# Kernel tuning notes

Measured on AMD Instinct MI355X. Metric: run time of the kernel, lower is better.

## Reference

```python
import jax, jax.numpy as jnp
import numpy as np

N = 4096
K = 64
E = N * K
LD = 2      # location_dim
ED = 8      # attention embed_dim
H = 256     # lck_structure width
BN_EPS = 1e-5


def setup_inputs() -> dict:
    key = jax.random.key(0)
    ks = jax.random.split(key, 12)
    coor = jax.random.normal(ks[0], (E, 2 * LD), dtype=jnp.float32)
    row = jnp.repeat(jnp.arange(N, dtype=jnp.int64), K)
    col = jax.random.randint(ks[1], (E,), 0, N, dtype=jnp.int64)
    sparse_idx = jnp.stack([row, col], axis=0)
    geodesic = jax.random.uniform(ks[2], (N, N), dtype=jnp.float32)
    angle_ratio = jax.random.uniform(ks[3], (N, N), dtype=jnp.float32)
    # LocalConditionalKer params: Linear(4,H), Linear(H,H), BN(H), Linear(H,1)
    W0 = jax.random.normal(ks[4], (2 * LD, H), dtype=jnp.float32) / np.sqrt(2 * LD)
    b0 = jnp.zeros((H,), jnp.float32)
    W1 = jax.random.normal(ks[5], (H, H), dtype=jnp.float32) / np.sqrt(H)
    b1 = jnp.zeros((H,), jnp.float32)
    gamma = jnp.ones((H,), jnp.float32)
    beta = jnp.zeros((H,), jnp.float32)
    W2 = jax.random.normal(ks[6], (H, 1), dtype=jnp.float32) / np.sqrt(H)
    b2 = jnp.zeros((1,), jnp.float32)
    # Attention params: query/key Linear(LD, ED)
    Wq = jax.random.normal(ks[7], (LD, ED), dtype=jnp.float32) / np.sqrt(LD)
    bq = jnp.zeros((ED,), jnp.float32)
    Wk = jax.random.normal(ks[8], (LD, ED), dtype=jnp.float32) / np.sqrt(LD)
    bk = jnp.zeros((ED,), jnp.float32)
    x = jax.random.normal(ks[9], (1,), dtype=jnp.float32)
    return dict(x=x, coor=coor, sparse_idx=sparse_idx, geodesic=geodesic,
                angle_ratio=angle_ratio, W0=W0, b0=b0, W1=W1, b1=b1,
                gamma=gamma, beta=beta, W2=W2, b2=b2,
                Wq=Wq, bq=bq, Wk=Wk, bk=bk)


def _lck(coor, W0, b0, W1, b1, gamma, beta, W2, b2):
    # loop semantics: activation applied before every layer except j==1
    h = jnp.tanh(coor) @ W0 + b0          # j=0: Linear(4,H)
    h = h @ W1 + b1                        # j=1: Linear(H,H), no pre-activation
    h = jnp.tanh(h)                        # j=2: BN(H) in training mode (batch stats)
    mu = jnp.mean(h, axis=0)
    var = jnp.var(h, axis=0)               # biased variance, as torch BN uses
    h = gamma * (h - mu) * jax.lax.rsqrt(var + BN_EPS) + beta
    h = jnp.tanh(h) @ W2 + b2              # j=3: Linear(H,1)
    return jax.nn.relu(h)                  # [E,1]


def reference(x, coor, sparse_idx, geodesic, angle_ratio,
              W0, b0, W1, b1, gamma, beta, W2, b2, Wq, bq, Wk, bk):
    row, col = sparse_idx[0], sparse_idx[1]
    # per-edge kernel value, scattered into dense NxN (duplicates summed)
    vals = _lck(coor, W0, b0, W1, b1, gamma, beta, W2, b2).reshape(-1)  # [E]
    lcker = jnp.zeros((N, N), vals.dtype).at[row, col].add(vals)
    # attention over neighbors
    sphere = coor[:, :LD] + coor[:, LD:]           # [E, 2]
    sphere = sphere.reshape(N, K, LD)               # [N, K, 2]
    center = sphere[:, :1, :]                       # [N, 1, 2]
    q = center @ Wq + bq                            # [N, 1, ED]
    k = sphere @ Wk + bk                            # [N, K, ED]
    att = jnp.abs(jnp.einsum('nqe,nke->nqk', q, k).squeeze(1))  # [N, K]
    alpha = jnp.zeros((N, N), att.dtype).at[row, col].add(att.reshape(-1))
    distance_decay = jnp.exp(-alpha * geodesic)
    return lcker * distance_decay * angle_ratio
```

## Files before the change

kernel.cpp:

```cpp
#include <hip/hip_runtime.h>

#define N_ 4096
#define K_ 64
#define E_ (N_*K_)
#define H_ 256
#define EPS_ 1e-5f
#define L2E_ 1.4426950408889634f
#define TL2E_ 2.8853900817779268f

#if __has_builtin(__builtin_amdgcn_exp2f)
#define EXP2(x) __builtin_amdgcn_exp2f(x)
#else
#define EXP2(x) __expf((x) * 0.6931471805599453f)
#endif

__device__ __forceinline__ float ftanh(float x) {
    float e = EXP2(x * TL2E_);
    return 1.0f - 2.0f * __builtin_amdgcn_rcpf(e + 1.0f);
}

__global__ __launch_bounds__(256) void prep_kernel(
    const float* __restrict__ W0, const float* __restrict__ b0,
    const float* __restrict__ W1, const float* __restrict__ b1,
    float* __restrict__ W01, float* __restrict__ b01)
{
    int c = threadIdx.x;
    int h0 = blockIdx.x * 8;
    float a0 = 0.f, a1 = 0.f, a2 = 0.f, a3 = 0.f, ab = 0.f;
    #pragma unroll
    for (int h = h0; h < h0 + 8; ++h) {
        float w = W1[h * H_ + c];
        a0 = fmaf(W0[0 * H_ + h], w, a0);
        a1 = fmaf(W0[1 * H_ + h], w, a1);
        a2 = fmaf(W0[2 * H_ + h], w, a2);
        a3 = fmaf(W0[3 * H_ + h], w, a3);
        ab = fmaf(b0[h], w, ab);
    }
    if (blockIdx.x == 0) ab += b1[c];
    atomicAdd(&W01[c], a0);
    atomicAdd(&W01[H_ + c], a1);
    atomicAdd(&W01[2 * H_ + c], a2);
    atomicAdd(&W01[3 * H_ + c], a3);
    atomicAdd(&b01[c], ab);
}

__global__ __launch_bounds__(256, 8) void stats_kernel(
    const float* __restrict__ coor, const float* __restrict__ W01,
    const float* __restrict__ b01, float* __restrict__ part)
{
    const int c = threadIdx.x;
    const float w0 = TL2E_ * W01[c],        w1 = TL2E_ * W01[H_ + c];
    const float w2 = TL2E_ * W01[2*H_ + c], w3 = TL2E_ * W01[3*H_ + c];
    const float bb = TL2E_ * b01[c];
    __shared__ float4 T[128];
    const int e0 = blockIdx.x * 128;
    if (c < 128) {
        float4 v = reinterpret_cast<const float4*>(coor)[e0 + c];
        T[c] = make_float4(ftanh(v.x), ftanh(v.y), ftanh(v.z), ftanh(v.w));
    }
    __syncthreads();
    float sr = 0.f, sr2 = 0.f;
    #pragma unroll 8
    for (int i = 0; i < 128; ++i) {
        float4 t = T[i];
        float u = fmaf(t.w, w3, fmaf(t.z, w2, fmaf(t.y, w1, fmaf(t.x, w0, bb))));
        float r = __builtin_amdgcn_rcpf(EXP2(u) + 1.0f);
        sr += r;
        sr2 = fmaf(r, r, sr2);
    }
    part[blockIdx.x * 512 + c] = sr;
    part[blockIdx.x * 512 + 256 + c] = sr2;
}

__global__ __launch_bounds__(512) void reduce_kernel(
    const float* __restrict__ part, float* __restrict__ sums)
{
    int t = threadIdx.x;
    int b0 = blockIdx.x * 64;
    float local = 0.f;
    #pragma unroll 8
    for (int b = b0; b < b0 + 64; ++b) local += part[b * 512 + t];
    atomicAdd(&sums[t], local);
}

__global__ __launch_bounds__(256) void finalize_kernel(
    const float* __restrict__ sums, const float* __restrict__ gamma,
    const float* __restrict__ beta, const float* __restrict__ W2,
    const float* __restrict__ b2,
    const float* __restrict__ W01, const float* __restrict__ b01,
    float* __restrict__ folded, float* __restrict__ swp)
{
    int c = threadIdx.x;
    const float inv = 1.0f / (float)E_;
    float p = sums[c] * inv;
    float q = sums[256 + c] * inv;
    float mu = 1.0f - 2.0f * p;
    float var = 4.0f * fmaf(-p, p, q);
    float a = gamma[c] * rsqrtf(var + EPS_);
    float bf = fmaf(-mu, a, beta[c]);
    folded[c * 8 + 0] = TL2E_ * W01[c];
    folded[c * 8 + 1] = TL2E_ * W01[H_ + c];
    folded[c * 8 + 2] = TL2E_ * W01[2 * H_ + c];
    folded[c * 8 + 3] = TL2E_ * W01[3 * H_ + c];
    folded[c * 8 + 4] = TL2E_ * b01[c];
    folded[c * 8 + 5] = -4.0f * L2E_ * a;
    folded[c * 8 + 6] = TL2E_ * (a + bf);
    folded[c * 8 + 7] = -2.0f * W2[c];
    __shared__ float red[256];
    red[c] = W2[c];
    __syncthreads();
    for (int s = 128; s > 0; s >>= 1) {
        if (c < s) red[c] += red[c + s];
        __syncthreads();
    }
    if (c == 0) swp[0] = red[0] + b2[0];
}

__global__ __launch_bounds__(256, 8) void edge_kernel(
    const float* __restrict__ coor, const int* __restrict__ idx,
    const float* __restrict__ folded, const float* __restrict__ swp,
    const float* __restrict__ Wq, const float* __restrict__ bq,
    const float* __restrict__ Wk, const float* __restrict__ bk,
    const float* __restrict__ geo, const float* __restrict__ ang,
    float* __restrict__ out)
{
    __shared__ float4 FS[2 * H_ + 16];
    __shared__ float  TSx[128], TSy[128], TSz[128], TSw[128];
    __shared__ float  ACC[16][128];
    __shared__ int    COL[128];
    __shared__ float  ATT[128];

    const int t = threadIdx.x;
    const int row0 = blockIdx.x * 2;
    const int eb0 = blockIdx.x * 128;

    {
        const float4* F = reinterpret_cast<const float4*>(folded);
        FS[t + (t >> 5)] = F[t];
        int j = t + 256;
        FS[j + (j >> 5)] = F[j];
    }
    int col = 0;
    if (t < 128) {
        float4 ce = reinterpret_cast<const float4*>(coor)[eb0 + t];
        TSx[t] = ftanh(ce.x); TSy[t] = ftanh(ce.y);
        TSz[t] = ftanh(ce.z); TSw[t] = ftanh(ce.w);
        col = idx[E_ + eb0 + t];
        float ex = ce.x + ce.z, ey = ce.y + ce.w;
        float sx = __shfl(ex, 0), sy = __shfl(ey, 0);
        float att = 0.f;
        #pragma unroll
        for (int j = 0; j < 8; ++j) {
            float qj = fmaf(sy, Wq[8 + j], fmaf(sx, Wq[j], bq[j]));
            float kj = fmaf(ey, Wk[8 + j], fmaf(ex, Wk[j], bk[j]));
            att = fmaf(qj, kj, att);
        }
        COL[t] = col;
        ATT[t] = fabsf(att);
    }
    {
        float4 z = make_float4(0.f, 0.f, 0.f, 0.f);
        float4* orow = reinterpret_cast<float4*>(out + (size_t)row0 * N_);
        #pragma unroll
        for (int i = 0; i < 8; ++i) orow[i * 256 + t] = z;
    }
    __syncthreads();

    const int eg = (t & 15) * 8;
    const int chunk = t >> 4;
    float4 xa = *reinterpret_cast<const float4*>(&TSx[eg]);
    float4 xb = *reinterpret_cast<const float4*>(&TSx[eg + 4]);
    float4 ya = *reinterpret_cast<const float4*>(&TSy[eg]);
    float4 yb = *reinterpret_cast<const float4*>(&TSy[eg + 4]);
    float4 za = *reinterpret_cast<const float4*>(&TSz[eg]);
    float4 zb = *reinterpret_cast<const float4*>(&TSz[eg + 4]);
    float4 wa = *reinterpret_cast<const float4*>(&TSw[eg]);
    float4 wb = *reinterpret_cast<const float4*>(&TSw[eg + 4]);
    const float4* Fp = &FS[chunk * 33];
    float ac0 = 0.f, ac1 = 0.f, ac2 = 0.f, ac3 = 0.f;
    float ac4 = 0.f, ac5 = 0.f, ac6 = 0.f, ac7 = 0.f;
    #define EVAL(tx_, ty_, tz_, tw_, ak) { \
        float u = fmaf(tw_, f0.w, fmaf(tz_, f0.z, fmaf(ty_, f0.y, fmaf(tx_, f0.x, f1.x)))); \
        float r = __builtin_amdgcn_rcpf(EXP2(u) + 1.0f); \
        float r2 = __builtin_amdgcn_rcpf(EXP2(fmaf(r, f1.y, f1.z)) + 1.0f); \
        ak = fmaf(r2, f1.w, ak); }
    #pragma unroll 4
    for (int i = 0; i < 16; ++i) {
        float4 f0 = Fp[2 * i];
        float4 f1 = Fp[2 * i + 1];
        EVAL(xa.x, ya.x, za.x, wa.x, ac0)
        EVAL(xa.y, ya.y, za.y, wa.y, ac1)
        EVAL(xa.z, ya.z, za.z, wa.z, ac2)
        EVAL(xa.w, ya.w, za.w, wa.w, ac3)
        EVAL(xb.x, yb.x, zb.x, wb.x, ac4)
        EVAL(xb.y, yb.y, zb.y, wb.y, ac5)
        EVAL(xb.z, yb.z, zb.z, wb.z, ac6)
        EVAL(xb.w, yb.w, zb.w, wb.w, ac7)
    }
    #undef EVAL
    *reinterpret_cast<float4*>(&ACC[chunk][eg])     = make_float4(ac0, ac1, ac2, ac3);
    *reinterpret_cast<float4*>(&ACC[chunk][eg + 4]) = make_float4(ac4, ac5, ac6, ac7);
    __syncthreads();

    const int w = t >> 6, lane = t & 63;
    if (w < 2) {
        float val = swp[0];
        #pragma unroll
        for (int c = 0; c < 16; ++c) val += ACC[c][t];
        val = fmaxf(val, 0.f);

        size_t p = (size_t)(row0 + w) * N_ + col;
        float g = geo[p], an = ang[p];

        const int rb = w * 64;
        unsigned long long m = 0;
        float asum = 0.f;
        #pragma unroll 8
        for (int j4 = 0; j4 < 16; ++j4) {
            int4   c4 = *reinterpret_cast<const int4*>(&COL[rb + 4 * j4]);
            float4 a4 = *reinterpret_cast<const float4*>(&ATT[rb + 4 * j4]);
            m |= (unsigned long long)(c4.x == col) << (4 * j4 + 0);
            m |= (unsigned long long)(c4.y == col) << (4 * j4 + 1);
            m |= (unsigned long long)(c4.z == col) << (4 * j4 + 2);
            m |= (unsigned long long)(c4.w == col) << (4 * j4 + 3);
            asum += (c4.x == col) ? a4.x : 0.f;
            asum += (c4.y == col) ? a4.y : 0.f;
            asum += (c4.z == col) ? a4.z : 0.f;
            asum += (c4.w == col) ? a4.w : 0.f;
        }
        bool leader = ((m & ((1ull << lane) - 1ull)) == 0ull);

        float vsum = val;
        unsigned long long m2 = m & ~(1ull << lane);
        while (__any(m2 != 0ull)) {
            unsigned long long pick = m2 ? m2 : 1ull;
            int j = __ffsll(pick) - 1;
            float bv = __shfl(val, j);
            if (m2) { vsum += bv; m2 &= m2 - 1; }
        }
        if (leader) {
            out[p] = vsum * __expf(-asum * g) * an;
        }
    }
}

extern "C" void kernel_launch(void* const* d_in, const int* in_sizes, int n_in,
                              void* d_out, int out_size, void* d_ws, size_t ws_size,
                              hipStream_t stream)
{
    const float* coor  = (const float*)d_in[1];
    const int*   idx   = (const int*)d_in[2];
    const float* geo   = (const float*)d_in[3];
    const float* ang   = (const float*)d_in[4];
    const float* W0    = (const float*)d_in[5];
    const float* b0    = (const float*)d_in[6];
    const float* W1    = (const float*)d_in[7];
    const float* b1    = (const float*)d_in[8];
    const float* gamma = (const float*)d_in[9];
    const float* beta  = (const float*)d_in[10];
    const float* W2    = (const float*)d_in[11];
    const float* b2    = (const float*)d_in[12];
    const float* Wq    = (const float*)d_in[13];
    const float* bq    = (const float*)d_in[14];
    const float* Wk    = (const float*)d_in[15];
    const float* bk    = (const float*)d_in[16];

    float* ws = (float*)d_ws;
    float* sums   = ws;
    float* W01    = ws + 512;
    float* b01    = ws + 1536;
    float* folded = ws + 1792;
    float* swp    = ws + 3840;
    float* part   = ws + 4096;

    hipMemsetAsync(ws, 0, 1792 * sizeof(float), stream);

    prep_kernel<<<32, 256, 0, stream>>>(W0, b0, W1, b1, W01, b01);
    stats_kernel<<<E_ / 128, 256, 0, stream>>>(coor, W01, b01, part);
    reduce_kernel<<<32, 512, 0, stream>>>(part, sums);
    finalize_kernel<<<1, 256, 0, stream>>>(sums, gamma, beta, W2, b2, W01, b01,
                                           folded, swp);
    edge_kernel<<<N_ / 2, 256, 0, stream>>>(coor, idx, folded, swp,
                                            Wq, bq, Wk, bk, geo, ang, (float*)d_out);
}
```

Baseline: 76.38 us.

## Collapse five launches and memset into three kernels with atomic partial sums

Replaces the memset, prep, reduce and finalize kernels. prep2 computes the folded W0·W1 weights without atomics, zeroes the 32 partial-sum buckets and reduces W2. stats_kernel now atomically accumulates its BN statistics into those 32 buckets, and every edge_kernel block re-reduces the buckets and computes the BN fold itself. This removes launch gaps and serial tiny kernels, in exchange for atomic contention in stats and redundant per-block reduction work in edge_kernel.

```diff
diff --git a/kernel.cpp b/kernel.cpp
--- a/kernel.cpp
+++ b/kernel.cpp
@@ -19,39 +19,68 @@
     return 1.0f - 2.0f * __builtin_amdgcn_rcpf(e + 1.0f);
 }
 
-__global__ __launch_bounds__(256) void prep_kernel(
+__global__ __launch_bounds__(256) void prep2_kernel(
     const float* __restrict__ W0, const float* __restrict__ b0,
     const float* __restrict__ W1, const float* __restrict__ b1,
-    float* __restrict__ W01, float* __restrict__ b01)
-{
-    int c = threadIdx.x;
-    int h0 = blockIdx.x * 8;
-    float a0 = 0.f, a1 = 0.f, a2 = 0.f, a3 = 0.f, ab = 0.f;
+    const float* __restrict__ W2, const float* __restrict__ b2,
+    float* __restrict__ W01g, float* __restrict__ swp, float* __restrict__ part)
+{
+    __shared__ float LW1[256 * 32];
+    __shared__ float W0s[5 * 256];
+    __shared__ float red[256];
+
+    const int t = threadIdx.x;
+    const int b = blockIdx.x;
+
     #pragma unroll
-    for (int h = h0; h < h0 + 8; ++h) {
-        float w = W1[h * H_ + c];
-        a0 = fmaf(W0[0 * H_ + h], w, a0);
-        a1 = fmaf(W0[1 * H_ + h], w, a1);
-        a2 = fmaf(W0[2 * H_ + h], w, a2);
-        a3 = fmaf(W0[3 * H_ + h], w, a3);
-        ab = fmaf(b0[h], w, ab);
-    }
-    if (blockIdx.x == 0) ab += b1[c];
-    atomicAdd(&W01[c], a0);
-    atomicAdd(&W01[H_ + c], a1);
-    atomicAdd(&W01[2 * H_ + c], a2);
-    atomicAdd(&W01[3 * H_ + c], a3);
-    atomicAdd(&b01[c], ab);
+    for (int k = 0; k < 8; ++k) part[b * 2048 + k * 256 + t] = 0.f;
+
+    {
+        const float4* W1_4 = reinterpret_cast<const float4*>(W1);
+        #pragma unroll
+        for (int k = 0; k < 8; ++k) {
+            int flat = k * 256 + t;
+            int h = flat >> 3, j = flat & 7;
+            *reinterpret_cast<float4*>(&LW1[h * 32 + 4 * j]) = W1_4[h * 64 + b * 8 + j];
+        }
+        W0s[t] = W0[t];
+        W0s[256 + t] = W0[256 + t];
+        W0s[512 + t] = W0[512 + t];
+        W0s[768 + t] = W0[768 + t];
+        W0s[1024 + t] = b0[t];
+        red[t] = W2[t];
+    }
+    __syncthreads();
+
+    const int role = t >> 5, c = t & 31;
+    if (role < 5) {
+        const float* wrow = &W0s[role * 256];
+        float acc = 0.f;
+        #pragma unroll 8
+        for (int h = 0; h < 256; ++h) acc = fmaf(wrow[h], LW1[h * 32 + c], acc);
+        int cg = b * 32 + c;
+        if (role < 4) W01g[role * 256 + cg] = TL2E_ * acc;
+        else          W01g[1024 + cg] = TL2E_ * (acc + b1[cg]);
+    }
+
+    if (b == 0) {
+        __syncthreads();
+        for (int s = 128; s > 0; s >>= 1) {
+            if (t < s) red[t] += red[t + s];
+            __syncthreads();
+        }
+        if (t == 0) swp[0] = red[0] + b2[0];
+    }
 }
 
 __global__ __launch_bounds__(256, 8) void stats_kernel(
-    const float* __restrict__ coor, const float* __restrict__ W01,
-    const float* __restrict__ b01, float* __restrict__ part)
+    const float* __restrict__ coor, const float* __restrict__ W01g,
+    float* __restrict__ part)
 {
     const int c = threadIdx.x;
-    const float w0 = TL2E_ * W01[c],        w1 = TL2E_ * W01[H_ + c];
-    const float w2 = TL2E_ * W01[2*H_ + c], w3 = TL2E_ * W01[3*H_ + c];
-    const float bb = TL2E_ * b01[c];
+    const float w0 = W01g[c],          w1 = W01g[H_ + c];
+    const float w2 = W01g[2 * H_ + c], w3 = W01g[3 * H_ + c];
+    const float bb = W01g[4 * H_ + c];
     __shared__ float4 T[128];
     const int e0 = blockIdx.x * 128;
     if (c < 128) {
@@ -68,57 +97,16 @@
         sr += r;
         sr2 = fmaf(r, r, sr2);
     }
-    part[blockIdx.x * 512 + c] = sr;
-    part[blockIdx.x * 512 + 256 + c] = sr2;
-}
-
-__global__ __launch_bounds__(512) void reduce_kernel(
-    const float* __restrict__ part, float* __restrict__ sums)
-{
-    int t = threadIdx.x;
-    int b0 = blockIdx.x * 64;
-    float local = 0.f;
-    #pragma unroll 8
-    for (int b = b0; b < b0 + 64; ++b) local += part[b * 512 + t];
-    atomicAdd(&sums[t], local);
-}
-
-__global__ __launch_bounds__(256) void finalize_kernel(
-    const float* __restrict__ sums, const float* __restrict__ gamma,
-    const float* __restrict__ beta, const float* __restrict__ W2,
-    const float* __restrict__ b2,
-    const float* __restrict__ W01, const float* __restrict__ b01,
-    float* __restrict__ folded, float* __restrict__ swp)
-{
-    int c = threadIdx.x;
-    const float inv = 1.0f / (float)E_;
-    float p = sums[c] * inv;
-    float q = sums[256 + c] * inv;
-    float mu = 1.0f - 2.0f * p;
-    float var = 4.0f * fmaf(-p, p, q);
-    float a = gamma[c] * rsqrtf(var + EPS_);
-    float bf = fmaf(-mu, a, beta[c]);
-    folded[c * 8 + 0] = TL2E_ * W01[c];
-    folded[c * 8 + 1] = TL2E_ * W01[H_ + c];
-    folded[c * 8 + 2] = TL2E_ * W01[2 * H_ + c];
-    folded[c * 8 + 3] = TL2E_ * W01[3 * H_ + c];
-    folded[c * 8 + 4] = TL2E_ * b01[c];
-    folded[c * 8 + 5] = -4.0f * L2E_ * a;
-    folded[c * 8 + 6] = TL2E_ * (a + bf);
-    folded[c * 8 + 7] = -2.0f * W2[c];
-    __shared__ float red[256];
-    red[c] = W2[c];
-    __syncthreads();
-    for (int s = 128; s > 0; s >>= 1) {
-        if (c < s) red[c] += red[c + s];
-        __syncthreads();
-    }
-    if (c == 0) swp[0] = red[0] + b2[0];
+    const int g = blockIdx.x & 31;
+    atomicAdd(&part[g * 512 + c], sr);
+    atomicAdd(&part[g * 512 + 256 + c], sr2);
 }
 
 __global__ __launch_bounds__(256, 8) void edge_kernel(
     const float* __restrict__ coor, const int* __restrict__ idx,
-    const float* __restrict__ folded, const float* __restrict__ swp,
+    const float* __restrict__ part, const float* __restrict__ W01g,
+    const float* __restrict__ gamma, const float* __restrict__ beta,
+    const float* __restrict__ W2, const float* __restrict__ swp,
     const float* __restrict__ Wq, const float* __restrict__ bq,
     const float* __restrict__ Wk, const float* __restrict__ bk,
     const float* __restrict__ geo, const float* __restrict__ ang,
@@ -135,10 +123,23 @@
     const int eb0 = blockIdx.x * 128;
 
     {
-        const float4* F = reinterpret_cast<const float4*>(folded);
-        FS[t + (t >> 5)] = F[t];
-        int j = t + 256;
-        FS[j + (j >> 5)] = F[j];
+        float sr = 0.f, sr2 = 0.f;
+        #pragma unroll 8
+        for (int g = 0; g < 32; ++g) {
+            sr  += part[g * 512 + t];
+            sr2 += part[g * 512 + 256 + t];
+        }
+        const float inv = 1.0f / (float)E_;
+        float sp = sr * inv;
+        float sq = sr2 * inv;
+        float mu = 1.0f - 2.0f * sp;
+        float var = 4.0f * fmaf(-sp, sp, sq);
+        float a  = gamma[t] * rsqrtf(var + EPS_);
+        float bf = fmaf(-mu, a, beta[t]);
+        int base = 2 * t + (t >> 4);
+        FS[base]     = make_float4(W01g[t], W01g[H_ + t], W01g[2 * H_ + t], W01g[3 * H_ + t]);
+        FS[base + 1] = make_float4(W01g[4 * H_ + t], -4.0f * L2E_ * a,
+                                   TL2E_ * (a + bf), -2.0f * W2[t]);
     }
     int col = 0;
     if (t < 128) {
@@ -265,21 +266,14 @@
     const float* Wk    = (const float*)d_in[15];
     const float* bk    = (const float*)d_in[16];
 
-    float* ws = (float*)d_ws;
-    float* sums   = ws;
-    float* W01    = ws + 512;
-    float* b01    = ws + 1536;
-    float* folded = ws + 1792;
-    float* swp    = ws + 3840;
-    float* part   = ws + 4096;
-
-    hipMemsetAsync(ws, 0, 1792 * sizeof(float), stream);
-
-    prep_kernel<<<32, 256, 0, stream>>>(W0, b0, W1, b1, W01, b01);
-    stats_kernel<<<E_ / 128, 256, 0, stream>>>(coor, W01, b01, part);
-    reduce_kernel<<<32, 512, 0, stream>>>(part, sums);
-    finalize_kernel<<<1, 256, 0, stream>>>(sums, gamma, beta, W2, b2, W01, b01,
-                                           folded, swp);
-    edge_kernel<<<N_ / 2, 256, 0, stream>>>(coor, idx, folded, swp,
-                                            Wq, bq, Wk, bk, geo, ang, (float*)d_out);
-}
+    float* ws   = (float*)d_ws;
+    float* swp  = ws;
+    float* W01g = ws + 256;
+    float* part = ws + 2048;
+
+    prep2_kernel<<<8, 256, 0, stream>>>(W0, b0, W1, b1, W2, b2, W01g, swp, part);
+    stats_kernel<<<E_ / 128, 256, 0, stream>>>(coor, W01g, part);
+    edge_kernel<<<N_ / 2, 256, 0, stream>>>(coor, idx, part, W01g, gamma, beta,
+                                            W2, swp, Wq, bq, Wk, bk, geo, ang,
+                                            (float*)d_out);
+}
```

Result: faster. 69.75 us (-8.7%).
